# Kernel tuning notes

Hardware: AMD Instinct MI355X
Metric: run time of the kernel (lower is better)

The kernel has to match this reference:

```python
import jax, jax.numpy as jnp
import numpy as np

N = 50000      # nodes
E = 800000     # edges per relation
R = 2          # relations
L = 2          # conv layers
D = 128        # hidden / input channels
G = 64         # graphs in batch
C = 8          # num_classes


def setup_inputs() -> dict:
    key = jax.random.key(0)
    ks = jax.random.split(key, 6)
    x = jax.random.normal(ks[0], (N, D), dtype=jnp.float32)
    W = jax.random.normal(ks[1], (L, R, D, D), dtype=jnp.float32) * 0.05
    b = jnp.zeros((L, R, D), dtype=jnp.float32)
    lin_w = jax.random.normal(ks[2], (D, C), dtype=jnp.float32) * 0.05
    lin_b = jnp.zeros((C,), dtype=jnp.float32)
    edge_index = jax.random.randint(ks[3], (R, 2, E), 0, N, dtype=jnp.int32)
    batch = jnp.sort(jax.random.randint(ks[4], (N,), 0, G, dtype=jnp.int32))
    return {"x": x, "W": W, "b": b, "lin_w": lin_w, "lin_b": lin_b,
            "edge_index": edge_index, "batch": batch}


def _gcn_conv(x, src, dst, inv_sqrt_deg, W_r, b_r):
    """PyG GCNConv: symmetric-normalized aggregation with self loops.
    out[i] = sum_{j->i} d_i^-1/2 d_j^-1/2 (x_j W) + d_i^-1 (x_i W) + b
    where d includes the self loop (in-degree + 1)."""
    xw = x @ W_r                                   # [N, D]
    norm = inv_sqrt_deg[src] * inv_sqrt_deg[dst]   # [E]
    agg = jax.ops.segment_sum(xw[src] * norm[:, None], dst, num_segments=N)
    agg = agg + xw * (inv_sqrt_deg * inv_sqrt_deg)[:, None]  # self-loop msg
    return agg + b_r


def reference(x, W, b, lin_w, lin_b, edge_index, batch):
    # Pre-compute per-relation symmetric normalization (same for all layers).
    inv_sqrt_degs = []
    for r in range(R):
        dst = edge_index[r, 1]
        deg = jax.ops.segment_sum(jnp.ones((E,), x.dtype), dst, num_segments=N) + 1.0
        inv_sqrt_degs.append(jax.lax.rsqrt(deg))

    h = x
    for l in range(L):
        out = jnp.zeros((N, D), x.dtype)
        for r in range(R):  # HeteroConv aggr='sum' over relations
            out = out + _gcn_conv(h, edge_index[r, 0], edge_index[r, 1],
                                  inv_sqrt_degs[r], W[l, r], b[l, r])
        h = jax.nn.relu(out) if l < L - 1 else out

    # global_mean_pool over batch ids
    counts = jax.ops.segment_sum(jnp.ones((N,), x.dtype), batch, num_segments=G)
    sums = jax.ops.segment_sum(h, batch, num_segments=G)
    pooled = sums / jnp.maximum(counts, 1.0)[:, None]   # [G, D]
    # dropout(p=0.5) is identity in eval mode; final Linear
    return pooled @ lin_w + lin_b                        # [G, C]
```

## Files before the change

### kernel.cpp

```cpp
#include <hip/hip_runtime.h>
#include <math.h>

#define NN 50000
#define EE 800000
#define RR 2
#define LL 2
#define DD 128
#define GG 64
#define CCLS 8
#define NBUK 196
#define BCAP 6144

typedef unsigned int uint;
typedef unsigned short ushort;
typedef short bf16x8 __attribute__((ext_vector_type(8)));
typedef float f32x4 __attribute__((ext_vector_type(4)));
typedef float f32x2 __attribute__((ext_vector_type(2)));

#define OFF_XW    ((size_t)0)
#define OFF_H1    ((size_t)12800000)
#define OFF_WBT   ((size_t)25600000)
#define OFF_ISD   ((size_t)25731072)
#define OFF_RP    ((size_t)26131072)
#define OFF_CI    ((size_t)26531136)
#define OFF_BD    ((size_t)32931136)
#define OFF_ZERO  ((size_t)42564928)
#define ZO_GCUR 0
#define ZO_SUM  1600
#define ZO_CNT  34368
#define ZERO_BYTES 34624

static __device__ __forceinline__ ushort f2b(float f) {
  uint u = __float_as_uint(f);
  uint r = (u + 0x7fffu + ((u >> 16) & 1u)) >> 16;
  return (ushort)r;
}
static __device__ __forceinline__ float blo(uint u) { return __uint_as_float(u << 16); }
static __device__ __forceinline__ float bhi(uint u) { return __uint_as_float(u & 0xffff0000u); }

__global__ __launch_bounds__(256) void k_wprep(const float* __restrict__ W,
                                               ushort* __restrict__ WT) {
  int idx = blockIdx.x * 256 + threadIdx.x;
  int lr = idx >> 14;
  int rem = idx & 16383;
  int n = rem >> 7, k = rem & 127;
  WT[lr * 16384 + n * 128 + k] = f2b(W[lr * 16384 + k * 128 + n]);
}

__global__ __launch_bounds__(256) void k_part(const int* __restrict__ EI,
                                              int* __restrict__ gcur,
                                              uint* __restrict__ bdata) {
  __shared__ int hist[256];
  __shared__ int sbase[256];
  __shared__ int gbase[256];
  __shared__ int lcur[256];
  __shared__ uint stage[4096];
  __shared__ unsigned char bstage[4096];
  const int r = blockIdx.y;
  const int t = threadIdx.x;
  const int e0 = blockIdx.x * 4096;
  const int cnt = min(4096, EE - e0);
  hist[t] = 0;
  lcur[t] = 0;
  __syncthreads();

  int src[16], dst[16];
  bool val[4];
#pragma unroll
  for (int j = 0; j < 4; ++j) {
    int i4 = (j * 256 + t) * 4;
    val[j] = (i4 < cnt);
    if (val[j]) {
      int4 s4 = *(const int4*)(EI + (size_t)r * 2 * EE + e0 + i4);
      int4 d4 = *(const int4*)(EI + (size_t)r * 2 * EE + EE + e0 + i4);
      src[j * 4 + 0] = s4.x; src[j * 4 + 1] = s4.y; src[j * 4 + 2] = s4.z; src[j * 4 + 3] = s4.w;
      dst[j * 4 + 0] = d4.x; dst[j * 4 + 1] = d4.y; dst[j * 4 + 2] = d4.z; dst[j * 4 + 3] = d4.w;
#pragma unroll
      for (int i = 0; i < 4; ++i) atomicAdd(&hist[dst[j * 4 + i] >> 8], 1);
    }
  }
  __syncthreads();
  int hv = hist[t];
  if (t < NBUK && hv > 0)
    gbase[t] = atomicAdd(&gcur[r * NBUK + t], hv);
  else
    gbase[t] = 0;
  sbase[t] = hv;
  __syncthreads();
  for (int off = 1; off < 256; off <<= 1) {
    int u = (t >= off) ? sbase[t - off] : 0;
    __syncthreads();
    sbase[t] += u;
    __syncthreads();
  }
  int incl = sbase[t];
  hist[t] = incl - hv;
  __syncthreads();
#pragma unroll
  for (int j = 0; j < 4; ++j) {
    if (val[j]) {
#pragma unroll
      for (int i = 0; i < 4; ++i) {
        int d = dst[j * 4 + i];
        int b = d >> 8;
        int p = atomicAdd(&lcur[b], 1);
        int pos = hist[b] + p;
        stage[pos] = ((uint)src[j * 4 + i] << 8) | (uint)(d & 255);
        bstage[pos] = (unsigned char)b;
      }
    }
  }
  __syncthreads();
  for (int s = t; s < cnt; s += 256) {
    int b = (int)bstage[s];
    bdata[(size_t)(r * NBUK + b) * BCAP + gbase[b] + (s - hist[b])] = stage[s];
  }
}

__global__ __launch_bounds__(256) void k_csr(const uint* __restrict__ bdata,
                                             const int* __restrict__ gcur,
                                             float* __restrict__ isd,
                                             int* __restrict__ rp,
                                             int* __restrict__ ci) {
  __shared__ int lcnt[256];
  __shared__ int lrp[256];
  __shared__ int lcur[256];
  __shared__ int cstage[BCAP];
  __shared__ int basesh;
  const int b = blockIdx.x;
  const int r = blockIdx.y;
  const int t = threadIdx.x;
  const int cnt = gcur[r * NBUK + b];
  lcnt[t] = (t < b) ? gcur[r * NBUK + t] : 0;
  __syncthreads();
  for (int off = 128; off > 0; off >>= 1) {
    if (t < off) lcnt[t] += lcnt[t + off];
    __syncthreads();
  }
  if (t == 0) basesh = lcnt[0];
  __syncthreads();
  const int base = basesh;
  const uint* bd = bdata + (size_t)(r * NBUK + b) * BCAP;
  __syncthreads();
  lcnt[t] = 0;
  lcur[t] = 0;
  __syncthreads();
  for (int s = t; s < cnt; s += 256) {
    uint pr = bd[s];
    atomicAdd(&lcnt[pr & 255u], 1);
  }
  __syncthreads();
  int deg = lcnt[t];
  lrp[t] = deg;
  __syncthreads();
  for (int off = 1; off < 256; off <<= 1) {
    int u = (t >= off) ? lrp[t - off] : 0;
    __syncthreads();
    lrp[t] += u;
    __syncthreads();
  }
  int incl = lrp[t];
  __syncthreads();
  lrp[t] = incl - deg;
  __syncthreads();
  int node = b * 256 + t;
  if (node < NN) {
    isd[r * NN + node] = rsqrtf((float)(deg + 1));
    rp[r * (NN + 1) + node] = base + lrp[t];
  }
  if (b == NBUK - 1 && t == 0) rp[r * (NN + 1) + NN] = EE;
  for (int s = t; s < cnt; s += 256) {
    uint pr = bd[s];
    int j = (int)(pr & 255u);
    int p = atomicAdd(&lcur[j], 1);
    cstage[lrp[j] + p] = (int)(pr >> 8);
  }
  __syncthreads();
  for (int s = t; s < cnt; s += 256) ci[(size_t)r * EE + base + s] = cstage[s];
}

#define AL_S 72
#define WT_S 136
template <int IN_BF16>
__global__ __launch_bounds__(256) void k_gemm(const void* __restrict__ Xv,
                                              const ushort* __restrict__ WTg,
                                              const float* __restrict__ isd,
                                              uint* __restrict__ Y) {
  __shared__ ushort WTl[128 * WT_S];
  __shared__ ushort Al[128 * AL_S];
  const int r = blockIdx.y;
  const int m0b = blockIdx.x * 128;
  const int t = threadIdx.x;
  const int w = t >> 6, L = t & 63, q = L >> 4, ln = L & 15;
  uint* Yr = Y + (size_t)r * NN * 32;
  const ushort* WTr = WTg + (size_t)r * 16384;

#pragma unroll
  for (int i = 0; i < 8; ++i) {
    int g = t + i * 256;
    int n = g >> 4, k0 = (g & 15) * 8;
    *(uint4*)(&WTl[n * WT_S + k0]) = *(const uint4*)(WTr + n * 128 + k0);
  }

  f32x4 acc[2][8];
#pragma unroll
  for (int mt = 0; mt < 2; ++mt)
#pragma unroll
    for (int nt = 0; nt < 8; ++nt) {
      acc[mt][nt][0] = 0.f; acc[mt][nt][1] = 0.f;
      acc[mt][nt][2] = 0.f; acc[mt][nt][3] = 0.f;
    }

  for (int hh = 0; hh < 2; ++hh) {
    __syncthreads();
    {
      int row = t >> 1, ch = t & 1;
      int gm = m0b + row;
      ushort* dst = &Al[row * AL_S + ch * 32];
      if (gm < NN) {
        if (IN_BF16) {
          const uint4* xp = (const uint4*)((const ushort*)Xv + (size_t)gm * 128 + hh * 64 + ch * 32);
#pragma unroll
          for (int j = 0; j < 4; ++j) ((uint4*)dst)[j] = xp[j];
        } else {
          const float4* xp = (const float4*)((const float*)Xv + (size_t)gm * 128 + hh * 64 + ch * 32);
          ushort tmp[32];
#pragma unroll
          for (int j = 0; j < 8; ++j) {
            float4 v = xp[j];
            tmp[j * 4 + 0] = f2b(v.x); tmp[j * 4 + 1] = f2b(v.y);
            tmp[j * 4 + 2] = f2b(v.z); tmp[j * 4 + 3] = f2b(v.w);
          }
#pragma unroll
          for (int j = 0; j < 4; ++j) ((uint4*)dst)[j] = ((uint4*)tmp)[j];
        }
      } else {
        uint4 z = make_uint4(0, 0, 0, 0);
#pragma unroll
        for (int j = 0; j < 4; ++j) ((uint4*)dst)[j] = z;
      }
    }
    __syncthreads();
#pragma unroll
    for (int kk = 0; kk < 2; ++kk) {
      bf16x8 b0 = *(const bf16x8*)(&Al[(w * 32 + ln) * AL_S + kk * 32 + q * 8]);
      bf16x8 b1 = *(const bf16x8*)(&Al[(w * 32 + 16 + ln) * AL_S + kk * 32 + q * 8]);
#pragma unroll
      for (int nt = 0; nt < 8; ++nt) {
        bf16x8 a = *(const bf16x8*)(&WTl[(nt * 16 + ln) * WT_S + hh * 64 + kk * 32 + q * 8]);
        acc[0][nt] = __builtin_amdgcn_mfma_f32_16x16x32_bf16(a, b0, acc[0][nt], 0, 0, 0);
        acc[1][nt] = __builtin_amdgcn_mfma_f32_16x16x32_bf16(a, b1, acc[1][nt], 0, 0, 0);
      }
    }
  }
#pragma unroll
  for (int mt = 0; mt < 2; ++mt) {
    int m = m0b + w * 32 + mt * 16 + ln;
    if (m < NN) {
      float sc = isd[r * NN + m];
      uint* yp = Yr + (size_t)m * 32;
#pragma unroll
      for (int nt = 0; nt < 8; ++nt) {
        f32x4 v = acc[mt][nt];
        uint u = __builtin_amdgcn_cvt_pk_fp8_f32(v[0] * sc, v[1] * sc, 0u, false);
        u = __builtin_amdgcn_cvt_pk_fp8_f32(v[2] * sc, v[3] * sc, u, true);
        yp[nt * 4 + q] = u;
      }
    }
  }
}

__global__ __launch_bounds__(256) void k_agg(const uint* __restrict__ xw,
                                             const int* __restrict__ rp,
                                             const int* __restrict__ ci,
                                             const float* __restrict__ isd,
                                             const float* __restrict__ bias,
                                             uint* __restrict__ hout, int relu_flag) {
  const int w = threadIdx.x >> 6;
  const int lane = threadIdx.x & 63;
  const int g = lane >> 3, c = lane & 7;
  const int i = blockIdx.x * 4 + w;

  f32x2 tot[8];
#pragma unroll
  for (int k = 0; k < 8; ++k) { tot[k][0] = 0.f; tot[k][1] = 0.f; }

#pragma unroll
  for (int r = 0; r < RR; ++r) {
    const char* xbase = (const char*)(xw + (size_t)r * NN * 32);
    const int* cir = ci + (size_t)r * EE;
    const float di = isd[r * NN + i];
    const int e0 = rp[r * (NN + 1) + i];
    const int cnt = rp[r * (NN + 1) + i + 1] - e0;
    const int total = cnt + 1;
    const uint coff = (uint)c * 16u;

    f32x2 acc[8];
#pragma unroll
    for (int k = 0; k < 8; ++k) { acc[k][0] = 0.f; acc[k][1] = 0.f; }

    int s_cur = (g < cnt) ? cir[e0 + g] : i;
    for (int base = 0; base < total; base += 8) {
      int idxn = base + 8 + g;
      int s_next = (idxn < cnt) ? cir[e0 + idxn] : i;
      if (base + g < total) {
        uint4 u = *(const uint4*)(xbase + ((uint)s_cur * 128u + coff));
        acc[0] += __builtin_amdgcn_cvt_pk_f32_fp8(u.x, false);
        acc[1] += __builtin_amdgcn_cvt_pk_f32_fp8(u.x, true);
        acc[2] += __builtin_amdgcn_cvt_pk_f32_fp8(u.y, false);
        acc[3] += __builtin_amdgcn_cvt_pk_f32_fp8(u.y, true);
        acc[4] += __builtin_amdgcn_cvt_pk_f32_fp8(u.z, false);
        acc[5] += __builtin_amdgcn_cvt_pk_f32_fp8(u.z, true);
        acc[6] += __builtin_amdgcn_cvt_pk_f32_fp8(u.w, false);
        acc[7] += __builtin_amdgcn_cvt_pk_f32_fp8(u.w, true);
      }
      s_cur = s_next;
    }
    f32x2 di2; di2[0] = di; di2[1] = di;
#pragma unroll
    for (int k = 0; k < 8; ++k) tot[k] += acc[k] * di2;
  }

  float* tf = (float*)tot;
#pragma unroll
  for (int mask = 8; mask <= 32; mask <<= 1) {
#pragma unroll
    for (int k = 0; k < 16; ++k) tf[k] += __shfl_xor(tf[k], mask);
  }

  if (g < 2) {
    int ch0 = c * 16 + g * 8;
    const float4* bp = (const float4*)(bias + ch0);
    const float4* bq = (const float4*)(bias + DD + ch0);
    float4 b0 = bp[0], b1 = bp[1], b2 = bq[0], b3 = bq[1];
    float o[8];
#pragma unroll
    for (int j = 0; j < 8; ++j) o[j] = (g == 0) ? tf[j] : tf[8 + j];
    o[0] += b0.x + b2.x; o[1] += b0.y + b2.y; o[2] += b0.z + b2.z; o[3] += b0.w + b2.w;
    o[4] += b1.x + b3.x; o[5] += b1.y + b3.y; o[6] += b1.z + b3.z; o[7] += b1.w + b3.w;
    if (relu_flag) {
#pragma unroll
      for (int j = 0; j < 8; ++j) o[j] = fmaxf(o[j], 0.f);
    }
    uint4 pk;
    pk.x = (uint)f2b(o[0]) | ((uint)f2b(o[1]) << 16);
    pk.y = (uint)f2b(o[2]) | ((uint)f2b(o[3]) << 16);
    pk.z = (uint)f2b(o[4]) | ((uint)f2b(o[5]) << 16);
    pk.w = (uint)f2b(o[6]) | ((uint)f2b(o[7]) << 16);
    ((uint4*)(hout + (size_t)i * 64))[c * 2 + g] = pk;
  }
}

#define PCHUNK 32
__global__ __launch_bounds__(64) void k_pool(const uint* __restrict__ h,
                                             const int* __restrict__ batch,
                                             float* __restrict__ sums,
                                             int* __restrict__ counts) {
  int lane = threadIdx.x;
  int n0 = blockIdx.x * PCHUNK;
  int n1 = n0 + PCHUNK;
  if (n1 > NN) n1 = NN;
  if (n0 >= NN) return;
  float aLo = 0.f, aHi = 0.f;
  int cnt = 0;
  int g = batch[n0];
  uint u = h[(size_t)n0 * 64 + lane];
  for (int n = n0; n < n1; ++n) {
    uint unext = 0;
    int gnext = g;
    if (n + 1 < n1) {
      unext = h[(size_t)(n + 1) * 64 + lane];
      gnext = batch[n + 1];
    }
    aLo += blo(u);
    aHi += bhi(u);
    cnt++;
    if (n + 1 < n1 && gnext != g) {
      atomicAdd(&sums[g * DD + lane * 2], aLo);
      atomicAdd(&sums[g * DD + lane * 2 + 1], aHi);
      if (lane == 0) atomicAdd(&counts[g], cnt);
      aLo = 0.f; aHi = 0.f; cnt = 0;
      g = gnext;
    }
    u = unext;
  }
  atomicAdd(&sums[g * DD + lane * 2], aLo);
  atomicAdd(&sums[g * DD + lane * 2 + 1], aHi);
  if (lane == 0) atomicAdd(&counts[g], cnt);
}

__global__ __launch_bounds__(512) void k_final(const float* __restrict__ sums,
                                               const int* __restrict__ counts,
                                               const float* __restrict__ lin_w,
                                               const float* __restrict__ lin_b,
                                               float* __restrict__ out) {
  int t = threadIdx.x;
  int g = t >> 3, co = t & 7;
  float cnt = (float)counts[g];
  if (cnt < 1.f) cnt = 1.f;
  float inv = 1.f / cnt;
  float v = lin_b[co];
  for (int d = 0; d < DD; ++d) v += (sums[g * DD + d] * inv) * lin_w[d * CCLS + co];
  out[t] = v;
}

extern "C" void kernel_launch(void* const* d_in, const int* in_sizes, int n_in,
                              void* d_out, int out_size, void* d_ws, size_t ws_size,
                              hipStream_t stream) {
  (void)in_sizes; (void)n_in; (void)out_size; (void)ws_size;
  const float* x     = (const float*)d_in[0];
  const float* W     = (const float*)d_in[1];
  const float* b     = (const float*)d_in[2];
  const float* lin_w = (const float*)d_in[3];
  const float* lin_b = (const float*)d_in[4];
  const int*   EI    = (const int*)d_in[5];
  const int*   batch = (const int*)d_in[6];
  float* out = (float*)d_out;

  char* ws = (char*)d_ws;
  uint*   xw    = (uint*)(ws + OFF_XW);
  uint*   h1    = (uint*)(ws + OFF_H1);
  ushort* WbfT  = (ushort*)(ws + OFF_WBT);
  float*  isd   = (float*)(ws + OFF_ISD);
  int*    rp    = (int*)(ws + OFF_RP);
  int*    ci    = (int*)(ws + OFF_CI);
  uint*   bdata = (uint*)(ws + OFF_BD);
  char*   zb    = ws + OFF_ZERO;
  int*    gcur  = (int*)(zb + ZO_GCUR);
  float*  sums  = (float*)(zb + ZO_SUM);
  int*    counts= (int*)(zb + ZO_CNT);

  (void)hipMemsetAsync(zb, 0, ZERO_BYTES, stream);

  k_wprep<<<256, 256, 0, stream>>>(W, WbfT);
  k_part<<<dim3((EE + 4095) / 4096, RR), 256, 0, stream>>>(EI, gcur, bdata);
  k_csr<<<dim3(NBUK, RR), 256, 0, stream>>>(bdata, gcur, isd, rp, ci);

  for (int l = 0; l < LL; ++l) {
    const ushort* WTl_g = WbfT + (size_t)l * RR * DD * DD;
    if (l == 0)
      k_gemm<0><<<dim3((NN + 127) / 128, RR), 256, 0, stream>>>((const void*)x, WTl_g, isd, xw);
    else
      k_gemm<1><<<dim3((NN + 127) / 128, RR), 256, 0, stream>>>((const void*)h1, WTl_g, isd, xw);
    k_agg<<<(NN + 3) / 4, 256, 0, stream>>>(xw, rp, ci, isd,
                                            b + (size_t)l * RR * DD, h1,
                                            (l < LL - 1) ? 1 : 0);
  }
  k_pool<<<(NN + PCHUNK - 1) / PCHUNK, 64, 0, stream>>>(h1, batch, sums, counts);
  k_final<<<1, GG * CCLS, 0, stream>>>(sums, counts, lin_w, lin_b, out);
}
```

Baseline: 259.6 us.

## Pad per-node neighbor lists to multiples of eight with dummy zero row

Builds a padded CSR in which each node's neighbor list, including its self-loop entry, is rounded up to a multiple of 8 and filled with a dummy index pointing at an extra zero row appended to the xw buffer. The aggregation loop then runs over whole 8-wide groups with no bounds checks or per-lane predicates, and reads a per-node start offset and group count instead of two row pointers. The cost is a larger index array, extra dummy gathers of the zero row, and a larger workspace layout.

```diff
diff --git a/kernel.cpp b/kernel.cpp
--- a/kernel.cpp
+++ b/kernel.cpp
@@ -10,6 +10,8 @@
 #define CCLS 8
 #define NBUK 196
 #define BCAP 6144
+#define PBCAP 8192
+#define CIPS (NBUK * PBCAP + 8)
 
 typedef unsigned int uint;
 typedef unsigned short ushort;
@@ -18,13 +20,14 @@
 typedef float f32x2 __attribute__((ext_vector_type(2)));
 
 #define OFF_XW    ((size_t)0)
-#define OFF_H1    ((size_t)12800000)
-#define OFF_WBT   ((size_t)25600000)
-#define OFF_ISD   ((size_t)25731072)
-#define OFF_RP    ((size_t)26131072)
-#define OFF_CI    ((size_t)26531136)
-#define OFF_BD    ((size_t)32931136)
-#define OFF_ZERO  ((size_t)42564928)
+#define OFF_H1    ((size_t)12800512)
+#define OFF_WBT   ((size_t)25600512)
+#define OFF_ISD   ((size_t)25731584)
+#define OFF_PRP   ((size_t)26131584)
+#define OFF_PNB   ((size_t)26531584)
+#define OFF_CIP   ((size_t)26731648)
+#define OFF_BD    ((size_t)39576832)
+#define OFF_ZERO  ((size_t)49210624)
 #define ZO_GCUR 0
 #define ZO_SUM  1600
 #define ZO_CNT  34368
@@ -39,12 +42,17 @@
 static __device__ __forceinline__ float bhi(uint u) { return __uint_as_float(u & 0xffff0000u); }
 
 __global__ __launch_bounds__(256) void k_wprep(const float* __restrict__ W,
-                                               ushort* __restrict__ WT) {
+                                               ushort* __restrict__ WT,
+                                               uint* __restrict__ xw) {
   int idx = blockIdx.x * 256 + threadIdx.x;
   int lr = idx >> 14;
   int rem = idx & 16383;
   int n = rem >> 7, k = rem & 127;
   WT[lr * 16384 + n * 128 + k] = f2b(W[lr * 16384 + k * 128 + n]);
+  if (blockIdx.x == 0 && threadIdx.x < 64) {
+    int rr = threadIdx.x >> 5, wd = threadIdx.x & 31;
+    xw[(size_t)rr * (NN + 1) * 32 + (size_t)NN * 32 + wd] = 0u;
+  }
 }
 
 __global__ __launch_bounds__(256) void k_part(const int* __restrict__ EI,
@@ -120,63 +128,56 @@
 __global__ __launch_bounds__(256) void k_csr(const uint* __restrict__ bdata,
                                              const int* __restrict__ gcur,
                                              float* __restrict__ isd,
-                                             int* __restrict__ rp,
-                                             int* __restrict__ ci) {
+                                             uint* __restrict__ prp,
+                                             ushort* __restrict__ pnb,
+                                             int* __restrict__ cip) {
   __shared__ int lcnt[256];
-  __shared__ int lrp[256];
+  __shared__ int ppos[256];
   __shared__ int lcur[256];
-  __shared__ int cstage[BCAP];
-  __shared__ int basesh;
+  __shared__ int pstage[PBCAP];
+  __shared__ int tot_sh;
   const int b = blockIdx.x;
   const int r = blockIdx.y;
   const int t = threadIdx.x;
   const int cnt = gcur[r * NBUK + b];
-  lcnt[t] = (t < b) ? gcur[r * NBUK + t] : 0;
-  __syncthreads();
-  for (int off = 128; off > 0; off >>= 1) {
-    if (t < off) lcnt[t] += lcnt[t + off];
-    __syncthreads();
-  }
-  if (t == 0) basesh = lcnt[0];
-  __syncthreads();
-  const int base = basesh;
   const uint* bd = bdata + (size_t)(r * NBUK + b) * BCAP;
-  __syncthreads();
   lcnt[t] = 0;
   lcur[t] = 0;
   __syncthreads();
-  for (int s = t; s < cnt; s += 256) {
-    uint pr = bd[s];
-    atomicAdd(&lcnt[pr & 255u], 1);
-  }
-  __syncthreads();
-  int deg = lcnt[t];
-  lrp[t] = deg;
+  for (int s = t; s < cnt; s += 256) atomicAdd(&lcnt[bd[s] & 255u], 1);
+  __syncthreads();
+  const int node = b * 256 + t;
+  const int deg = lcnt[t];
+  const int pdeg = (node < NN) ? ((deg + 8) & ~7) : 0;
+  ppos[t] = pdeg;
   __syncthreads();
   for (int off = 1; off < 256; off <<= 1) {
-    int u = (t >= off) ? lrp[t - off] : 0;
-    __syncthreads();
-    lrp[t] += u;
-    __syncthreads();
-  }
-  int incl = lrp[t];
-  __syncthreads();
-  lrp[t] = incl - deg;
-  __syncthreads();
-  int node = b * 256 + t;
+    int u = (t >= off) ? ppos[t - off] : 0;
+    __syncthreads();
+    ppos[t] += u;
+    __syncthreads();
+  }
+  if (t == 255) tot_sh = ppos[255];
+  int excl = ppos[t] - pdeg;
+  __syncthreads();
+  ppos[t] = excl;
+  __syncthreads();
   if (node < NN) {
     isd[r * NN + node] = rsqrtf((float)(deg + 1));
-    rp[r * (NN + 1) + node] = base + lrp[t];
-  }
-  if (b == NBUK - 1 && t == 0) rp[r * (NN + 1) + NN] = EE;
+    prp[r * NN + node] = (uint)(b * PBCAP + excl);
+    pnb[r * NN + node] = (ushort)(pdeg >> 3);
+    pstage[excl + deg] = node;
+    for (int s = deg + 1; s < pdeg; ++s) pstage[excl + s] = NN;
+  }
   for (int s = t; s < cnt; s += 256) {
     uint pr = bd[s];
     int j = (int)(pr & 255u);
     int p = atomicAdd(&lcur[j], 1);
-    cstage[lrp[j] + p] = (int)(pr >> 8);
-  }
-  __syncthreads();
-  for (int s = t; s < cnt; s += 256) ci[(size_t)r * EE + base + s] = cstage[s];
+    pstage[ppos[j] + p] = (int)(pr >> 8);
+  }
+  __syncthreads();
+  const int ptot = tot_sh;
+  for (int s = t; s < ptot; s += 256) cip[(size_t)r * CIPS + b * PBCAP + s] = pstage[s];
 }
 
 #define AL_S 72
@@ -192,7 +193,7 @@
   const int m0b = blockIdx.x * 128;
   const int t = threadIdx.x;
   const int w = t >> 6, L = t & 63, q = L >> 4, ln = L & 15;
-  uint* Yr = Y + (size_t)r * NN * 32;
+  uint* Yr = Y + (size_t)r * (NN + 1) * 32;
   const ushort* WTr = WTg + (size_t)r * 16384;
 
 #pragma unroll
@@ -271,8 +272,9 @@
 }
 
 __global__ __launch_bounds__(256) void k_agg(const uint* __restrict__ xw,
-                                             const int* __restrict__ rp,
-                                             const int* __restrict__ ci,
+                                             const uint* __restrict__ prp,
+                                             const ushort* __restrict__ pnb,
+                                             const int* __restrict__ cip,
                                              const float* __restrict__ isd,
                                              const float* __restrict__ bias,
                                              uint* __restrict__ hout, int relu_flag) {
@@ -287,33 +289,28 @@
 
 #pragma unroll
   for (int r = 0; r < RR; ++r) {
-    const char* xbase = (const char*)(xw + (size_t)r * NN * 32);
-    const int* cir = ci + (size_t)r * EE;
+    const char* xb = (const char*)xw + (size_t)r * (NN + 1) * 128;
+    const int* ip = cip + (size_t)r * CIPS + prp[r * NN + i] + g;
+    const int nb = (int)pnb[r * NN + i];
     const float di = isd[r * NN + i];
-    const int e0 = rp[r * (NN + 1) + i];
-    const int cnt = rp[r * (NN + 1) + i + 1] - e0;
-    const int total = cnt + 1;
     const uint coff = (uint)c * 16u;
 
     f32x2 acc[8];
 #pragma unroll
     for (int k = 0; k < 8; ++k) { acc[k][0] = 0.f; acc[k][1] = 0.f; }
 
-    int s_cur = (g < cnt) ? cir[e0 + g] : i;
-    for (int base = 0; base < total; base += 8) {
-      int idxn = base + 8 + g;
-      int s_next = (idxn < cnt) ? cir[e0 + idxn] : i;
-      if (base + g < total) {
-        uint4 u = *(const uint4*)(xbase + ((uint)s_cur * 128u + coff));
-        acc[0] += __builtin_amdgcn_cvt_pk_f32_fp8(u.x, false);
-        acc[1] += __builtin_amdgcn_cvt_pk_f32_fp8(u.x, true);
-        acc[2] += __builtin_amdgcn_cvt_pk_f32_fp8(u.y, false);
-        acc[3] += __builtin_amdgcn_cvt_pk_f32_fp8(u.y, true);
-        acc[4] += __builtin_amdgcn_cvt_pk_f32_fp8(u.z, false);
-        acc[5] += __builtin_amdgcn_cvt_pk_f32_fp8(u.z, true);
-        acc[6] += __builtin_amdgcn_cvt_pk_f32_fp8(u.w, false);
-        acc[7] += __builtin_amdgcn_cvt_pk_f32_fp8(u.w, true);
-      }
+    int s_cur = ip[0];
+    for (int bq = 1; bq <= nb; ++bq) {
+      int s_next = ip[bq * 8];
+      uint4 u = *(const uint4*)(xb + ((uint)s_cur * 128u + coff));
+      acc[0] += __builtin_amdgcn_cvt_pk_f32_fp8(u.x, false);
+      acc[1] += __builtin_amdgcn_cvt_pk_f32_fp8(u.x, true);
+      acc[2] += __builtin_amdgcn_cvt_pk_f32_fp8(u.y, false);
+      acc[3] += __builtin_amdgcn_cvt_pk_f32_fp8(u.y, true);
+      acc[4] += __builtin_amdgcn_cvt_pk_f32_fp8(u.z, false);
+      acc[5] += __builtin_amdgcn_cvt_pk_f32_fp8(u.z, true);
+      acc[6] += __builtin_amdgcn_cvt_pk_f32_fp8(u.w, false);
+      acc[7] += __builtin_amdgcn_cvt_pk_f32_fp8(u.w, true);
       s_cur = s_next;
     }
     f32x2 di2; di2[0] = di; di2[1] = di;
@@ -422,8 +419,9 @@
   uint*   h1    = (uint*)(ws + OFF_H1);
   ushort* WbfT  = (ushort*)(ws + OFF_WBT);
   float*  isd   = (float*)(ws + OFF_ISD);
-  int*    rp    = (int*)(ws + OFF_RP);
-  int*    ci    = (int*)(ws + OFF_CI);
+  uint*   prp   = (uint*)(ws + OFF_PRP);
+  ushort* pnb   = (ushort*)(ws + OFF_PNB);
+  int*    cip   = (int*)(ws + OFF_CIP);
   uint*   bdata = (uint*)(ws + OFF_BD);
   char*   zb    = ws + OFF_ZERO;
   int*    gcur  = (int*)(zb + ZO_GCUR);
@@ -432,9 +430,9 @@
 
   (void)hipMemsetAsync(zb, 0, ZERO_BYTES, stream);
 
-  k_wprep<<<256, 256, 0, stream>>>(W, WbfT);
+  k_wprep<<<256, 256, 0, stream>>>(W, WbfT, xw);
   k_part<<<dim3((EE + 4095) / 4096, RR), 256, 0, stream>>>(EI, gcur, bdata);
-  k_csr<<<dim3(NBUK, RR), 256, 0, stream>>>(bdata, gcur, isd, rp, ci);
+  k_csr<<<dim3(NBUK, RR), 256, 0, stream>>>(bdata, gcur, isd, prp, pnb, cip);
 
   for (int l = 0; l < LL; ++l) {
     const ushort* WTl_g = WbfT + (size_t)l * RR * DD * DD;
@@ -442,7 +440,7 @@
       k_gemm<0><<<dim3((NN + 127) / 128, RR), 256, 0, stream>>>((const void*)x, WTl_g, isd, xw);
     else
       k_gemm<1><<<dim3((NN + 127) / 128, RR), 256, 0, stream>>>((const void*)h1, WTl_g, isd, xw);
-    k_agg<<<(NN + 3) / 4, 256, 0, stream>>>(xw, rp, ci, isd,
+    k_agg<<<(NN + 3) / 4, 256, 0, stream>>>(xw, prp, pnb, cip, isd,
                                             b + (size_t)l * RR * DD, h1,
                                             (l < LL - 1) ? 1 : 0);
   }
```

Measured after the change: 265.0 us. 2.1% more time.

## Load each A tile once for both relations; fuse pooling with final linear

Applied to the files above, without the earlier changes.

The GEMM kernel now loads the full 128x128 input tile into shared memory once and loops over both relations inside the block, reloading only the weight tile. This halves the input reads and cuts the grid to one dimension. The pooling and final linear layer are merged into one kernel with one block per graph. Each block finds its node range by binary search over the sorted batch array, so the atomics, the zeroed sums buffer and one launch go away. The pooled kernel has only 64 blocks, each streaming roughly 780 nodes serially, which could limit parallelism compared to the previous chunked atomic version.

```diff
diff --git a/kernel.cpp b/kernel.cpp
--- a/kernel.cpp
+++ b/kernel.cpp
@@ -23,12 +23,8 @@
 #define OFF_ISD   ((size_t)25731072)
 #define OFF_RP    ((size_t)26131072)
 #define OFF_CI    ((size_t)26531136)
-#define OFF_BD    ((size_t)32931136)
-#define OFF_ZERO  ((size_t)42564928)
-#define ZO_GCUR 0
-#define ZO_SUM  1600
-#define ZO_CNT  34368
-#define ZERO_BYTES 34624
+#define OFF_BD    ((size_t)32931200)
+#define OFF_GCUR  ((size_t)42564992)
 
 static __device__ __forceinline__ ushort f2b(float f) {
   uint u = __float_as_uint(f);
@@ -179,92 +175,93 @@
   for (int s = t; s < cnt; s += 256) ci[(size_t)r * EE + base + s] = cstage[s];
 }
 
-#define AL_S 72
-#define WT_S 136
+#define TS 136
 template <int IN_BF16>
 __global__ __launch_bounds__(256) void k_gemm(const void* __restrict__ Xv,
                                               const ushort* __restrict__ WTg,
                                               const float* __restrict__ isd,
                                               uint* __restrict__ Y) {
-  __shared__ ushort WTl[128 * WT_S];
-  __shared__ ushort Al[128 * AL_S];
-  const int r = blockIdx.y;
+  __shared__ ushort WTl[128 * TS];
+  __shared__ ushort Al[128 * TS];
   const int m0b = blockIdx.x * 128;
   const int t = threadIdx.x;
   const int w = t >> 6, L = t & 63, q = L >> 4, ln = L & 15;
-  uint* Yr = Y + (size_t)r * NN * 32;
-  const ushort* WTr = WTg + (size_t)r * 16384;
-
-#pragma unroll
-  for (int i = 0; i < 8; ++i) {
-    int g = t + i * 256;
-    int n = g >> 4, k0 = (g & 15) * 8;
-    *(uint4*)(&WTl[n * WT_S + k0]) = *(const uint4*)(WTr + n * 128 + k0);
-  }
-
-  f32x4 acc[2][8];
-#pragma unroll
-  for (int mt = 0; mt < 2; ++mt)
-#pragma unroll
-    for (int nt = 0; nt < 8; ++nt) {
-      acc[mt][nt][0] = 0.f; acc[mt][nt][1] = 0.f;
-      acc[mt][nt][2] = 0.f; acc[mt][nt][3] = 0.f;
-    }
-
+
+#pragma unroll
   for (int hh = 0; hh < 2; ++hh) {
+    int row = t >> 1, ch = t & 1;
+    int gm = m0b + row;
+    ushort* dst = &Al[row * TS + hh * 64 + ch * 32];
+    if (gm < NN) {
+      if (IN_BF16) {
+        const uint4* xp = (const uint4*)((const ushort*)Xv + (size_t)gm * 128 + hh * 64 + ch * 32);
+#pragma unroll
+        for (int j = 0; j < 4; ++j) ((uint4*)dst)[j] = xp[j];
+      } else {
+        const float4* xp = (const float4*)((const float*)Xv + (size_t)gm * 128 + hh * 64 + ch * 32);
+        ushort tmp[32];
+#pragma unroll
+        for (int j = 0; j < 8; ++j) {
+          float4 v = xp[j];
+          tmp[j * 4 + 0] = f2b(v.x); tmp[j * 4 + 1] = f2b(v.y);
+          tmp[j * 4 + 2] = f2b(v.z); tmp[j * 4 + 3] = f2b(v.w);
+        }
+#pragma unroll
+        for (int j = 0; j < 4; ++j) ((uint4*)dst)[j] = ((uint4*)tmp)[j];
+      }
+    } else {
+      uint4 z = make_uint4(0, 0, 0, 0);
+#pragma unroll
+      for (int j = 0; j < 4; ++j) ((uint4*)dst)[j] = z;
+    }
+  }
+
+  for (int r = 0; r < RR; ++r) {
     __syncthreads();
     {
-      int row = t >> 1, ch = t & 1;
-      int gm = m0b + row;
-      ushort* dst = &Al[row * AL_S + ch * 32];
-      if (gm < NN) {
-        if (IN_BF16) {
-          const uint4* xp = (const uint4*)((const ushort*)Xv + (size_t)gm * 128 + hh * 64 + ch * 32);
-#pragma unroll
-          for (int j = 0; j < 4; ++j) ((uint4*)dst)[j] = xp[j];
-        } else {
-          const float4* xp = (const float4*)((const float*)Xv + (size_t)gm * 128 + hh * 64 + ch * 32);
-          ushort tmp[32];
-#pragma unroll
-          for (int j = 0; j < 8; ++j) {
-            float4 v = xp[j];
-            tmp[j * 4 + 0] = f2b(v.x); tmp[j * 4 + 1] = f2b(v.y);
-            tmp[j * 4 + 2] = f2b(v.z); tmp[j * 4 + 3] = f2b(v.w);
-          }
-#pragma unroll
-          for (int j = 0; j < 4; ++j) ((uint4*)dst)[j] = ((uint4*)tmp)[j];
-        }
-      } else {
-        uint4 z = make_uint4(0, 0, 0, 0);
-#pragma unroll
-        for (int j = 0; j < 4; ++j) ((uint4*)dst)[j] = z;
-      }
-    }
-    __syncthreads();
-#pragma unroll
-    for (int kk = 0; kk < 2; ++kk) {
-      bf16x8 b0 = *(const bf16x8*)(&Al[(w * 32 + ln) * AL_S + kk * 32 + q * 8]);
-      bf16x8 b1 = *(const bf16x8*)(&Al[(w * 32 + 16 + ln) * AL_S + kk * 32 + q * 8]);
+      const ushort* WTr = WTg + (size_t)r * 16384;
+#pragma unroll
+      for (int i = 0; i < 8; ++i) {
+        int g = t + i * 256;
+        int n = g >> 4, k0 = (g & 15) * 8;
+        *(uint4*)(&WTl[n * TS + k0]) = *(const uint4*)(WTr + n * 128 + k0);
+      }
+    }
+    __syncthreads();
+
+    f32x4 acc[2][8];
+#pragma unroll
+    for (int mt = 0; mt < 2; ++mt)
 #pragma unroll
       for (int nt = 0; nt < 8; ++nt) {
-        bf16x8 a = *(const bf16x8*)(&WTl[(nt * 16 + ln) * WT_S + hh * 64 + kk * 32 + q * 8]);
+        acc[mt][nt][0] = 0.f; acc[mt][nt][1] = 0.f;
+        acc[mt][nt][2] = 0.f; acc[mt][nt][3] = 0.f;
+      }
+#pragma unroll
+    for (int kk = 0; kk < 4; ++kk) {
+      bf16x8 b0 = *(const bf16x8*)(&Al[(w * 32 + ln) * TS + kk * 32 + q * 8]);
+      bf16x8 b1 = *(const bf16x8*)(&Al[(w * 32 + 16 + ln) * TS + kk * 32 + q * 8]);
+#pragma unroll
+      for (int nt = 0; nt < 8; ++nt) {
+        bf16x8 a = *(const bf16x8*)(&WTl[(nt * 16 + ln) * TS + kk * 32 + q * 8]);
         acc[0][nt] = __builtin_amdgcn_mfma_f32_16x16x32_bf16(a, b0, acc[0][nt], 0, 0, 0);
         acc[1][nt] = __builtin_amdgcn_mfma_f32_16x16x32_bf16(a, b1, acc[1][nt], 0, 0, 0);
       }
     }
-  }
-#pragma unroll
-  for (int mt = 0; mt < 2; ++mt) {
-    int m = m0b + w * 32 + mt * 16 + ln;
-    if (m < NN) {
-      float sc = isd[r * NN + m];
-      uint* yp = Yr + (size_t)m * 32;
-#pragma unroll
-      for (int nt = 0; nt < 8; ++nt) {
-        f32x4 v = acc[mt][nt];
-        uint u = __builtin_amdgcn_cvt_pk_fp8_f32(v[0] * sc, v[1] * sc, 0u, false);
-        u = __builtin_amdgcn_cvt_pk_fp8_f32(v[2] * sc, v[3] * sc, u, true);
-        yp[nt * 4 + q] = u;
+    uint* Yr = Y + (size_t)r * NN * 32;
+#pragma unroll
+    for (int mt = 0; mt < 2; ++mt) {
+      int m = m0b + w * 32 + mt * 16 + ln;
+      if (m < NN) {
+        float sc = isd[r * NN + m];
+        uint* yp = Yr + (size_t)m * 32;
+#pragma unroll
+        for (int nt = 0; nt < 8; ++nt) {
+          f32x4 v = acc[mt][nt];
+          uint u = __builtin_amdgcn_cvt_pk_fp8_f32(v[0] * sc, v[1] * sc, 0u, false);
+          u = __builtin_amdgcn_cvt_pk_fp8_f32(v[2] * sc, v[3] * sc, u, true);
+          yp[nt * 4 + q] = u;
+        }
       }
     }
   }
@@ -351,57 +348,55 @@
   }
 }
 
-#define PCHUNK 32
-__global__ __launch_bounds__(64) void k_pool(const uint* __restrict__ h,
-                                             const int* __restrict__ batch,
-                                             float* __restrict__ sums,
-                                             int* __restrict__ counts) {
-  int lane = threadIdx.x;
-  int n0 = blockIdx.x * PCHUNK;
-  int n1 = n0 + PCHUNK;
-  if (n1 > NN) n1 = NN;
-  if (n0 >= NN) return;
+__global__ __launch_bounds__(64) void k_poolfinal(const uint* __restrict__ h,
+                                                  const int* __restrict__ batch,
+                                                  const float* __restrict__ lin_w,
+                                                  const float* __restrict__ lin_b,
+                                                  float* __restrict__ out) {
+  const int g = blockIdx.x;
+  const int lane = threadIdx.x;
+  int lo = 0, hi2 = NN;
+  while (lo < hi2) { int mid = (lo + hi2) >> 1; if (batch[mid] < g) lo = mid + 1; else hi2 = mid; }
+  int hi = lo, hh = NN;
+  while (hi < hh) { int mid = (hi + hh) >> 1; if (batch[mid] < g + 1) hi = mid + 1; else hh = mid; }
+
   float aLo = 0.f, aHi = 0.f;
-  int cnt = 0;
-  int g = batch[n0];
-  uint u = h[(size_t)n0 * 64 + lane];
-  for (int n = n0; n < n1; ++n) {
-    uint unext = 0;
-    int gnext = g;
-    if (n + 1 < n1) {
-      unext = h[(size_t)(n + 1) * 64 + lane];
-      gnext = batch[n + 1];
-    }
+  int n = lo;
+  for (; n + 4 <= hi; n += 4) {
+    uint u0 = h[(size_t)(n + 0) * 64 + lane];
+    uint u1 = h[(size_t)(n + 1) * 64 + lane];
+    uint u2 = h[(size_t)(n + 2) * 64 + lane];
+    uint u3 = h[(size_t)(n + 3) * 64 + lane];
+    aLo += blo(u0) + blo(u1) + blo(u2) + blo(u3);
+    aHi += bhi(u0) + bhi(u1) + bhi(u2) + bhi(u3);
+  }
+  for (; n < hi; ++n) {
+    uint u = h[(size_t)n * 64 + lane];
     aLo += blo(u);
     aHi += bhi(u);
-    cnt++;
-    if (n + 1 < n1 && gnext != g) {
-      atomicAdd(&sums[g * DD + lane * 2], aLo);
-      atomicAdd(&sums[g * DD + lane * 2 + 1], aHi);
-      if (lane == 0) atomicAdd(&counts[g], cnt);
-      aLo = 0.f; aHi = 0.f; cnt = 0;
-      g = gnext;
-    }
-    u = unext;
-  }
-  atomicAdd(&sums[g * DD + lane * 2], aLo);
-  atomicAdd(&sums[g * DD + lane * 2 + 1], aHi);
-  if (lane == 0) atomicAdd(&counts[g], cnt);
-}
-
-__global__ __launch_bounds__(512) void k_final(const float* __restrict__ sums,
-                                               const int* __restrict__ counts,
-                                               const float* __restrict__ lin_w,
-                                               const float* __restrict__ lin_b,
-                                               float* __restrict__ out) {
-  int t = threadIdx.x;
-  int g = t >> 3, co = t & 7;
-  float cnt = (float)counts[g];
-  if (cnt < 1.f) cnt = 1.f;
-  float inv = 1.f / cnt;
-  float v = lin_b[co];
-  for (int d = 0; d < DD; ++d) v += (sums[g * DD + d] * inv) * lin_w[d * CCLS + co];
-  out[t] = v;
+  }
+  int cnt = hi - lo;
+  float inv = 1.f / (float)max(cnt, 1);
+  float mLo = aLo * inv, mHi = aHi * inv;
+
+  const int d0 = lane * 2;
+  float p[CCLS];
+  const float4* w0 = (const float4*)(lin_w + d0 * CCLS);
+  const float4* w1 = (const float4*)(lin_w + (d0 + 1) * CCLS);
+  float4 a0 = w0[0], a1 = w0[1], c0 = w1[0], c1 = w1[1];
+  p[0] = mLo * a0.x + mHi * c0.x; p[1] = mLo * a0.y + mHi * c0.y;
+  p[2] = mLo * a0.z + mHi * c0.z; p[3] = mLo * a0.w + mHi * c0.w;
+  p[4] = mLo * a1.x + mHi * c1.x; p[5] = mLo * a1.y + mHi * c1.y;
+  p[6] = mLo * a1.z + mHi * c1.z; p[7] = mLo * a1.w + mHi * c1.w;
+#pragma unroll
+  for (int mask = 1; mask <= 32; mask <<= 1) {
+#pragma unroll
+    for (int cc = 0; cc < CCLS; ++cc) p[cc] += __shfl_xor(p[cc], mask);
+  }
+  if (lane == 0) {
+#pragma unroll
+    for (int cc = 0; cc < CCLS; ++cc) out[g * CCLS + cc] = p[cc] + lin_b[cc];
+  }
 }
 
 extern "C" void kernel_launch(void* const* d_in, const int* in_sizes, int n_in,
@@ -425,12 +420,9 @@
   int*    rp    = (int*)(ws + OFF_RP);
   int*    ci    = (int*)(ws + OFF_CI);
   uint*   bdata = (uint*)(ws + OFF_BD);
-  char*   zb    = ws + OFF_ZERO;
-  int*    gcur  = (int*)(zb + ZO_GCUR);
-  float*  sums  = (float*)(zb + ZO_SUM);
-  int*    counts= (int*)(zb + ZO_CNT);
-
-  (void)hipMemsetAsync(zb, 0, ZERO_BYTES, stream);
+  int*    gcur  = (int*)(ws + OFF_GCUR);
+
+  (void)hipMemsetAsync(gcur, 0, 1600, stream);
 
   k_wprep<<<256, 256, 0, stream>>>(W, WbfT);
   k_part<<<dim3((EE + 4095) / 4096, RR), 256, 0, stream>>>(EI, gcur, bdata);
@@ -439,13 +431,12 @@
   for (int l = 0; l < LL; ++l) {
     const ushort* WTl_g = WbfT + (size_t)l * RR * DD * DD;
     if (l == 0)
-      k_gemm<0><<<dim3((NN + 127) / 128, RR), 256, 0, stream>>>((const void*)x, WTl_g, isd, xw);
+      k_gemm<0><<<(NN + 127) / 128, 256, 0, stream>>>((const void*)x, WTl_g, isd, xw);
     else
-      k_gemm<1><<<dim3((NN + 127) / 128, RR), 256, 0, stream>>>((const void*)h1, WTl_g, isd, xw);
+      k_gemm<1><<<(NN + 127) / 128, 256, 0, stream>>>((const void*)h1, WTl_g, isd, xw);
     k_agg<<<(NN + 3) / 4, 256, 0, stream>>>(xw, rp, ci, isd,
                                             b + (size_t)l * RR * DD, h1,
                                             (l < LL - 1) ? 1 : 0);
   }
-  k_pool<<<(NN + PCHUNK - 1) / PCHUNK, 64, 0, stream>>>(h1, batch, sums, counts);
-  k_final<<<1, GG * CCLS, 0, stream>>>(sums, counts, lin_w, lin_b, out);
-}
+  k_poolfinal<<<GG, 64, 0, stream>>>(h1, batch, lin_w, lin_b, out);
+}
```

Result: slower. 305.6 us (+17.7%).
